# Performance work log

Measured on AMD Instinct MI355X. Metric: run time of the kernel, lower is better.

## Reference

```python
import jax, jax.numpy as jnp
import numpy as np

N = 50000
E = 600000
D = 128


def gcn_conv(x, row, col, w, W, b):
    """PyG GCNConv: add self-loops (weight 1), symmetric deg^-1/2 normalization,
    linear transform, edge-weighted scatter-add aggregation, then bias."""
    n = x.shape[0]
    loop = jnp.arange(n)
    r = jnp.concatenate([row, loop])            # source nodes, [E+N]
    c = jnp.concatenate([col, loop])            # target nodes, [E+N]
    ww = jnp.concatenate([w, jnp.ones((n,), x.dtype)])
    deg = jax.ops.segment_sum(ww, c, num_segments=n)          # weighted in-degree
    dinv = jnp.where(deg > 0, jax.lax.rsqrt(deg), jnp.zeros_like(deg))
    norm = dinv[r] * ww * dinv[c]               # [E+N]
    xl = x @ W                                  # [n, D_out]
    msg = norm[:, None] * xl[r]                 # gather + scale, [E+N, D_out]
    out = jax.ops.segment_sum(msg, c, num_segments=n)
    return out + b


def setup_inputs() -> dict:
    key = jax.random.key(0)
    ks = jax.random.split(key, 12)
    x = jax.random.normal(ks[0], (N, D), dtype=jnp.float32)
    edge_index = jax.random.randint(ks[1], (2, E), 0, N, dtype=jnp.int64)
    edge_weights = jax.random.uniform(ks[2], (E,), dtype=jnp.float32)
    s = 1.0 / np.sqrt(D)
    W1 = jax.random.uniform(ks[3], (D, D), jnp.float32, -s, s)
    b1 = jnp.zeros((D,), jnp.float32)
    W2 = jax.random.uniform(ks[4], (D, D), jnp.float32, -s, s)
    b2 = jnp.zeros((D,), jnp.float32)
    W3 = jax.random.uniform(ks[5], (D, D), jnp.float32, -s, s)
    b3 = jnp.zeros((D,), jnp.float32)
    prelu_w = jnp.array(0.25, jnp.float32)
    return {"x": x, "edge_index": edge_index, "edge_weights": edge_weights,
            "W1": W1, "b1": b1, "W2": W2, "b2": b2, "W3": W3, "b3": b3,
            "prelu_w": prelu_w}


def reference(x, edge_index, edge_weights, W1, b1, W2, b2, W3, b3, prelu_w):
    row, col = edge_index[0], edge_index[1]
    # layer 1: GCNConv -> (dropout: eval, identity) -> ELU
    h = gcn_conv(x, row, col, edge_weights, W1, b1)
    h = jax.nn.elu(h)
    # layer 2: GCNConv -> GELU (torch default = exact erf)
    h = gcn_conv(h, row, col, edge_weights, W2, b2)
    h = jax.nn.gelu(h, approximate=False)
    # layer 3: GCNConv -> PReLU (learnable scalar slope)
    h = gcn_conv(h, row, col, edge_weights, W3, b3)
    h = jnp.where(h >= 0, h, prelu_w * h)
    return h
```

## Files before the change

### kernel.cpp

```cpp
#include <hip/hip_runtime.h>
#include <hip/hip_fp16.h>
#include <math.h>

constexpr int D = 128;

struct __align__(16) H8 { __half2 h[4]; };
struct __align__(8)  H4 { __half2 a, b; };

typedef _Float16 half8 __attribute__((ext_vector_type(8)));
typedef float    floatx4 __attribute__((ext_vector_type(4)));


__device__ __forceinline__ int detect64(const int* __restrict__ ei) {
  int z = 0;
#pragma unroll
  for (int i = 0; i < 8; ++i) z |= ei[2 * i + 1];
  return (z == 0) ? 1 : 0;
}

__device__ __forceinline__ void load_edge(const int* __restrict__ ei, int e, int nE,
                                          int m64, int n, int& r, int& c) {
  if (m64) { r = ei[2 * (size_t)e]; c = ei[2 * ((size_t)nE + e)]; }
  else     { r = ei[(size_t)e];     c = ei[(size_t)nE + e]; }
  r = min(max(r, 0), n - 1);
  c = min(max(c, 0), n - 1);
}

__global__ void k_zero(int* __restrict__ cnt, int n) {
  int i = blockIdx.x * blockDim.x + threadIdx.x;
  if (i < n) cnt[i] = 0;
}

__global__ void k_pos(const int* __restrict__ ei, int* __restrict__ cnt,
                      int2* __restrict__ rc, int* __restrict__ pos, int nE, int n) {
  int e = blockIdx.x * blockDim.x + threadIdx.x;
  if (e >= nE) return;
  int m64 = detect64(ei);
  int r, c;
  load_edge(ei, e, nE, m64, n, r, c);
  rc[e] = make_int2(r, c);
  pos[e] = atomicAdd(&cnt[c], 1);
}

__global__ void k_scan1(const int* __restrict__ cnt, int* __restrict__ offs,
                        int* __restrict__ bsum, int n) {
  __shared__ int s[256];
  int t = threadIdx.x;
  int i = blockIdx.x * 256 + t;
  int v = (i < n) ? cnt[i] : 0;
  s[t] = v;
  __syncthreads();
  for (int off = 1; off < 256; off <<= 1) {
    int x = 0;
    if (t >= off) x = s[t - off];
    __syncthreads();
    if (t >= off) s[t] += x;
    __syncthreads();
  }
  if (i < n) offs[i] = s[t] - v;
  if (t == 255) bsum[blockIdx.x] = s[255];
}

__global__ void k_scan2(const int* __restrict__ bsum, int* __restrict__ boff, int nb) {
  __shared__ int s[256];
  int t = threadIdx.x;
  int v = (t < nb) ? bsum[t] : 0;
  s[t] = v;
  __syncthreads();
  for (int off = 1; off < 256; off <<= 1) {
    int x = 0;
    if (t >= off) x = s[t - off];
    __syncthreads();
    if (t >= off) s[t] += x;
    __syncthreads();
  }
  if (t < nb) boff[t] = s[t] - v;
}

__global__ void k_scan3(int* __restrict__ offs, const int* __restrict__ boff, int n, int nE) {
  int i = blockIdx.x * 256 + threadIdx.x;
  if (i < n) offs[i] += boff[blockIdx.x];
  if (i == 0) offs[n] = nE;
}

__global__ void k_fill(const int2* __restrict__ rc, const int* __restrict__ pos,
                       const float* __restrict__ w, const int* __restrict__ offs,
                       int2* __restrict__ ecf, int nE) {
  int e = blockIdx.x * blockDim.x + threadIdx.x;
  if (e >= nE) return;
  int2 p = rc[e];
  int idx = offs[p.y] + pos[e];
  ecf[idx] = make_int2(p.x, __float_as_int(w[e]));
}

__global__ void k_degdinv(const int2* __restrict__ ecf, const int* __restrict__ offs,
                          float* __restrict__ dinv, int n) {
  int i = blockIdx.x * blockDim.x + threadIdx.x;
  if (i >= n) return;
  float s = 1.0f;
  int e1 = offs[i + 1];
  for (int e = offs[i]; e < e1; ++e) s += __int_as_float(ecf[e].y);
  dinv[i] = rsqrtf(s);
}

__global__ void k_coef(const int2* __restrict__ ecf, const float* __restrict__ dinv,
                       unsigned int* __restrict__ ecf2, int nE) {
  int e = blockIdx.x * blockDim.x + threadIdx.x;
  if (e >= nE) return;
  int2 p = ecf[e];
  float c = dinv[p.x] * __int_as_float(p.y);
  ecf2[e] = ((unsigned int)p.x << 16) |
            (unsigned int)__half_as_ushort(__float2half_rn(c));
}

__global__ void k_wt(const float* __restrict__ W1, const float* __restrict__ W2,
                     const float* __restrict__ W3, __half* __restrict__ Wt) {
  __shared__ float s[128][129];
  const float* W = blockIdx.x == 0 ? W1 : (blockIdx.x == 1 ? W2 : W3);
  __half* o = Wt + (size_t)blockIdx.x * D * D;
  int tid = threadIdx.x;
#pragma unroll
  for (int i = 0; i < 16; ++i) {
    int flat = i * 1024 + tid * 4;
    int k = flat >> 7;
    int nn = flat & 127;
    float4 v = *(const float4*)(W + (size_t)k * D + nn);
    s[k][nn] = v.x; s[k][nn + 1] = v.y; s[k][nn + 2] = v.z; s[k][nn + 3] = v.w;
  }
  __syncthreads();
#pragma unroll
  for (int i = 0; i < 8; ++i) {
    int flat = i * 256 + tid;
    int nn = flat >> 4;
    int k0 = (flat & 15) * 8;
    H8 hv;
#pragma unroll
    for (int t = 0; t < 4; ++t)
      hv.h[t] = __floats2half2_rn(s[k0 + 2 * t][nn], s[k0 + 2 * t + 1][nn]);
    *(H8*)(o + (size_t)nn * D + k0) = hv;
  }
}

template <int ACT>
__device__ __forceinline__ float act_f(float x) {
  if (ACT == 1) return x > 0.f ? x : expm1f(x);
  if (ACT == 2) return 0.5f * x * (1.0f + erff(x * 0.70710678118654752440f));
  return x;
}

template <int ACT, typename AT>
__global__ __launch_bounds__(256) void k_gemm(const AT* __restrict__ A,
                                              const __half* __restrict__ Wt,
                                              __half* __restrict__ Y, int n) {
  const int wave = threadIdx.x >> 6;
  const int lane = threadIdx.x & 63;
  const int np = lane & 15;
  const int quad = lane >> 4;
  const int node = blockIdx.x * 64 + wave * 16 + np;
  const int nc = min(node, n - 1);

  half8 b[4];
#pragma unroll
  for (int s = 0; s < 4; ++s) {
    if constexpr (sizeof(AT) == 4) {
      const float* ap = (const float*)A + (size_t)nc * D + s * 32 + quad * 8;
      float4 v0 = *(const float4*)ap;
      float4 v1 = *(const float4*)(ap + 4);
      b[s][0] = (_Float16)act_f<ACT>(v0.x); b[s][1] = (_Float16)act_f<ACT>(v0.y);
      b[s][2] = (_Float16)act_f<ACT>(v0.z); b[s][3] = (_Float16)act_f<ACT>(v0.w);
      b[s][4] = (_Float16)act_f<ACT>(v1.x); b[s][5] = (_Float16)act_f<ACT>(v1.y);
      b[s][6] = (_Float16)act_f<ACT>(v1.z); b[s][7] = (_Float16)act_f<ACT>(v1.w);
    } else {
      half8 raw = *(const half8*)((const __half*)A + (size_t)nc * D + s * 32 + quad * 8);
#pragma unroll
      for (int t = 0; t < 8; ++t)
        b[s][t] = (_Float16)act_f<ACT>((float)raw[t]);
    }
  }

  floatx4 acc[8];
#pragma unroll
  for (int mt = 0; mt < 8; ++mt) acc[mt] = (floatx4){0.f, 0.f, 0.f, 0.f};

#pragma unroll
  for (int mt = 0; mt < 8; ++mt) {
#pragma unroll
    for (int s = 0; s < 4; ++s) {
      half8 a = *(const half8*)(Wt + (size_t)(mt * 16 + np) * D + s * 32 + quad * 8);
      acc[mt] = __builtin_amdgcn_mfma_f32_16x16x32_f16(a, b[s], acc[mt], 0, 0, 0);
    }
  }

  if (node < n) {
#pragma unroll
    for (int mt = 0; mt < 8; ++mt) {
      H4 hv;
      hv.a = __floats2half2_rn(acc[mt][0], acc[mt][1]);
      hv.b = __floats2half2_rn(acc[mt][2], acc[mt][3]);
      *(H4*)(Y + (size_t)node * D + mt * 16 + quad * 4) = hv;
    }
  }
}

__device__ __forceinline__ void fmacc8(float* acc, float c, const H8& y) {
  float2 f;
  f = __half22float2(y.h[0]); acc[0] += c * f.x; acc[1] += c * f.y;
  f = __half22float2(y.h[1]); acc[2] += c * f.x; acc[3] += c * f.y;
  f = __half22float2(y.h[2]); acc[4] += c * f.x; acc[5] += c * f.y;
  f = __half22float2(y.h[3]); acc[6] += c * f.x; acc[7] += c * f.y;
}

__device__ __forceinline__ float cdecode(unsigned int u) {
  return __half2float(__ushort_as_half((unsigned short)(u & 0xffffu)));
}

template <int PRELU, typename OutT>
__global__ __launch_bounds__(256) void k_agg(const __half* __restrict__ Y,
                                             const int* __restrict__ offs,
                                             const unsigned int* __restrict__ ecf2,
                                             const float* __restrict__ dinv,
                                             const float* __restrict__ bias,
                                             const float* __restrict__ pw,
                                             OutT* __restrict__ OUT, int n) {
  int gi = blockIdx.x * blockDim.x + threadIdx.x;
  int node = gi >> 5;
  int sub = (gi >> 4) & 1;
  int j = gi & 15;
  if (node >= n) return;
  float dc = dinv[node];
  float acc[8] = {0.f, 0.f, 0.f, 0.f, 0.f, 0.f, 0.f, 0.f};
  if (sub == 0) {
    H8 ys = *(const H8*)(Y + (size_t)node * D + j * 8);
    fmacc8(acc, dc, ys);
  }
  int e0 = offs[node], e1 = offs[node + 1];
  int e = e0 + sub;
  for (; e + 6 < e1; e += 8) {
    unsigned int u0 = ecf2[e], u1 = ecf2[e + 2], u2 = ecf2[e + 4], u3 = ecf2[e + 6];
    H8 y0 = *(const H8*)(Y + (size_t)(u0 >> 16) * D + j * 8);
    H8 y1 = *(const H8*)(Y + (size_t)(u1 >> 16) * D + j * 8);
    H8 y2 = *(const H8*)(Y + (size_t)(u2 >> 16) * D + j * 8);
    H8 y3 = *(const H8*)(Y + (size_t)(u3 >> 16) * D + j * 8);
    fmacc8(acc, cdecode(u0), y0);
    fmacc8(acc, cdecode(u1), y1);
    fmacc8(acc, cdecode(u2), y2);
    fmacc8(acc, cdecode(u3), y3);
  }
  for (; e < e1; e += 2) {
    unsigned int u = ecf2[e];
    H8 y = *(const H8*)(Y + (size_t)(u >> 16) * D + j * 8);
    fmacc8(acc, cdecode(u), y);
  }
#pragma unroll
  for (int i = 0; i < 8; ++i) acc[i] += __shfl_xor(acc[i], 16, 64);
  float4 b4 = *(const float4*)(bias + j * 8 + sub * 4);
  float o[4];
  o[0] = dc * acc[sub * 4 + 0] + b4.x;
  o[1] = dc * acc[sub * 4 + 1] + b4.y;
  o[2] = dc * acc[sub * 4 + 2] + b4.z;
  o[3] = dc * acc[sub * 4 + 3] + b4.w;
  if (PRELU) {
    float wv = *pw;
#pragma unroll
    for (int i = 0; i < 4; ++i) o[i] = o[i] >= 0.f ? o[i] : wv * o[i];
  }
  if constexpr (sizeof(OutT) == 4) {
    *(float4*)((float*)OUT + (size_t)node * D + j * 8 + sub * 4) =
        make_float4(o[0], o[1], o[2], o[3]);
  } else {
    H4 hv;
    hv.a = __floats2half2_rn(o[0], o[1]);
    hv.b = __floats2half2_rn(o[2], o[3]);
    *(H4*)((__half*)OUT + (size_t)node * D + j * 8 + sub * 4) = hv;
  }
}

extern "C" void kernel_launch(void* const* d_in, const int* in_sizes, int n_in,
                              void* d_out, int out_size, void* d_ws, size_t ws_size,
                              hipStream_t stream) {
  const float* x  = (const float*)d_in[0];
  const int*   ei = (const int*)d_in[1];
  const float* w  = (const float*)d_in[2];
  const float* W1 = (const float*)d_in[3];
  const float* b1 = (const float*)d_in[4];
  const float* W2 = (const float*)d_in[5];
  const float* b2 = (const float*)d_in[6];
  const float* W3 = (const float*)d_in[7];
  const float* b3 = (const float*)d_in[8];
  const float* pw = (const float*)d_in[9];
  const int N = in_sizes[0] / D;
  const int E = in_sizes[2];
  float* out = (float*)d_out;

  char* wsb = (char*)d_ws;
  size_t off = 0;
  auto alloc = [&](size_t bytes) {
    void* p = wsb + off;
    off = (off + bytes + 255) & ~(size_t)255;
    return p;
  };
  float*        dinv = (float*)alloc((size_t)N * 4);
  int*          cnt  = (int*)alloc((size_t)N * 4);
  int*          offs = (int*)alloc((size_t)(N + 1) * 4);
  int*          bsum = (int*)alloc(256 * 4);
  int*          boff = (int*)alloc(256 * 4);
  int2*         ecf  = (int2*)alloc((size_t)E * 8);
  unsigned int* ecf2 = (unsigned int*)alloc((size_t)E * 4);
  __half*       Wt   = (__half*)alloc((size_t)3 * D * D * 2);
  __half*       Y    = (__half*)alloc((size_t)N * D * 2);
  __half*       h    = (__half*)alloc((size_t)N * D * 2);
  int2*         rc   = (int2*)Y;
  int*          pos  = (int*)((char*)Y + (size_t)E * 8);

  const int nb = (N + 255) / 256;
  const int eb = (E + 255) / 256;

  hipLaunchKernelGGL(k_wt,      dim3(3),  dim3(256), 0, stream, W1, W2, W3, Wt);
  hipLaunchKernelGGL(k_zero,    dim3(nb), dim3(256), 0, stream, cnt, N);
  hipLaunchKernelGGL(k_pos,     dim3(eb), dim3(256), 0, stream, ei, cnt, rc, pos, E, N);
  hipLaunchKernelGGL(k_scan1,   dim3(nb), dim3(256), 0, stream, cnt, offs, bsum, N);
  hipLaunchKernelGGL(k_scan2,   dim3(1),  dim3(256), 0, stream, bsum, boff, nb);
  hipLaunchKernelGGL(k_scan3,   dim3(nb), dim3(256), 0, stream, offs, boff, N, E);
  hipLaunchKernelGGL(k_fill,    dim3(eb), dim3(256), 0, stream, rc, pos, w, offs, ecf, E);
  hipLaunchKernelGGL(k_degdinv, dim3(nb), dim3(256), 0, stream, ecf, offs, dinv, N);
  hipLaunchKernelGGL(k_coef,    dim3(eb), dim3(256), 0, stream, ecf, dinv, ecf2, E);

  const int gb = (N + 63) / 64;
  const int ab = (N * 32 + 255) / 256;

  hipLaunchKernelGGL((k_gemm<0, float>),  dim3(gb), dim3(256), 0, stream, x, Wt,             Y, N);
  hipLaunchKernelGGL((k_agg<0, __half>),  dim3(ab), dim3(256), 0, stream, Y, offs, ecf2, dinv, b1, pw, h, N);
  hipLaunchKernelGGL((k_gemm<1, __half>), dim3(gb), dim3(256), 0, stream, h, Wt + D * D,     Y, N);
  hipLaunchKernelGGL((k_agg<0, __half>),  dim3(ab), dim3(256), 0, stream, Y, offs, ecf2, dinv, b2, pw, h, N);
  hipLaunchKernelGGL((k_gemm<2, __half>), dim3(gb), dim3(256), 0, stream, h, Wt + 2 * D * D, Y, N);
  hipLaunchKernelGGL((k_agg<1, float>),   dim3(ab), dim3(256), 0, stream, Y, offs, ecf2, dinv, b3, pw, out, N);
}
```

Baseline: 307.4 us.

## Split feature matrices into 32-column chunks for cache-friendly aggregation

Stores the transformed features Y and the hidden activations h in a chunked layout of four 32-feature slabs, each holding all nodes. Each aggregation block now handles one chunk for 32 nodes, so the random gathers in a block touch only one 3.2 MB slab instead of the whole 12.8 MB matrix. The aim is better L2 hit rate on the gather-heavy aggregation. In exchange, edge indices and coefficients are reread four times, and each gathered row is only 64 bytes.

```diff
diff --git a/kernel.cpp b/kernel.cpp
--- a/kernel.cpp
+++ b/kernel.cpp
@@ -171,7 +171,7 @@
       b[s][4] = (_Float16)act_f<ACT>(v1.x); b[s][5] = (_Float16)act_f<ACT>(v1.y);
       b[s][6] = (_Float16)act_f<ACT>(v1.z); b[s][7] = (_Float16)act_f<ACT>(v1.w);
     } else {
-      half8 raw = *(const half8*)((const __half*)A + (size_t)nc * D + s * 32 + quad * 8);
+      half8 raw = *(const half8*)((const __half*)A + ((size_t)s * n + nc) * 32 + quad * 8);
 #pragma unroll
       for (int t = 0; t < 8; ++t)
         b[s][t] = (_Float16)act_f<ACT>((float)raw[t]);
@@ -197,7 +197,8 @@
       H4 hv;
       hv.a = __floats2half2_rn(acc[mt][0], acc[mt][1]);
       hv.b = __floats2half2_rn(acc[mt][2], acc[mt][3]);
-      *(H4*)(Y + (size_t)node * D + mt * 16 + quad * 4) = hv;
+      int f0 = mt * 16 + quad * 4;
+      *(H4*)(Y + ((size_t)(f0 >> 5) * n + node) * 32 + (f0 & 31)) = hv;
     }
   }
 }
@@ -222,25 +223,27 @@
                                              const float* __restrict__ bias,
                                              const float* __restrict__ pw,
                                              OutT* __restrict__ OUT, int n) {
-  int gi = blockIdx.x * blockDim.x + threadIdx.x;
-  int node = gi >> 5;
-  int sub = (gi >> 4) & 1;
-  int j = gi & 15;
+  const int chunk = blockIdx.x & 3;
+  const int t = threadIdx.x;
+  const int node = (blockIdx.x >> 2) * 32 + (t >> 3);
+  const int sub = (t >> 2) & 1;
+  const int j = t & 3;
   if (node >= n) return;
+  const __half* Yc = Y + (size_t)chunk * n * 32;
   float dc = dinv[node];
   float acc[8] = {0.f, 0.f, 0.f, 0.f, 0.f, 0.f, 0.f, 0.f};
   if (sub == 0) {
-    H8 ys = *(const H8*)(Y + (size_t)node * D + j * 8);
+    H8 ys = *(const H8*)(Yc + (size_t)node * 32 + j * 8);
     fmacc8(acc, dc, ys);
   }
   int e0 = offs[node], e1 = offs[node + 1];
   int e = e0 + sub;
   for (; e + 6 < e1; e += 8) {
     unsigned int u0 = ecf2[e], u1 = ecf2[e + 2], u2 = ecf2[e + 4], u3 = ecf2[e + 6];
-    H8 y0 = *(const H8*)(Y + (size_t)(u0 >> 16) * D + j * 8);
-    H8 y1 = *(const H8*)(Y + (size_t)(u1 >> 16) * D + j * 8);
-    H8 y2 = *(const H8*)(Y + (size_t)(u2 >> 16) * D + j * 8);
-    H8 y3 = *(const H8*)(Y + (size_t)(u3 >> 16) * D + j * 8);
+    H8 y0 = *(const H8*)(Yc + (size_t)(u0 >> 16) * 32 + j * 8);
+    H8 y1 = *(const H8*)(Yc + (size_t)(u1 >> 16) * 32 + j * 8);
+    H8 y2 = *(const H8*)(Yc + (size_t)(u2 >> 16) * 32 + j * 8);
+    H8 y3 = *(const H8*)(Yc + (size_t)(u3 >> 16) * 32 + j * 8);
     fmacc8(acc, cdecode(u0), y0);
     fmacc8(acc, cdecode(u1), y1);
     fmacc8(acc, cdecode(u2), y2);
@@ -248,12 +251,12 @@
   }
   for (; e < e1; e += 2) {
     unsigned int u = ecf2[e];
-    H8 y = *(const H8*)(Y + (size_t)(u >> 16) * D + j * 8);
+    H8 y = *(const H8*)(Yc + (size_t)(u >> 16) * 32 + j * 8);
     fmacc8(acc, cdecode(u), y);
   }
 #pragma unroll
-  for (int i = 0; i < 8; ++i) acc[i] += __shfl_xor(acc[i], 16, 64);
-  float4 b4 = *(const float4*)(bias + j * 8 + sub * 4);
+  for (int i = 0; i < 8; ++i) acc[i] += __shfl_xor(acc[i], 4, 64);
+  float4 b4 = *(const float4*)(bias + chunk * 32 + j * 8 + sub * 4);
   float o[4];
   o[0] = dc * acc[sub * 4 + 0] + b4.x;
   o[1] = dc * acc[sub * 4 + 1] + b4.y;
@@ -265,13 +268,13 @@
     for (int i = 0; i < 4; ++i) o[i] = o[i] >= 0.f ? o[i] : wv * o[i];
   }
   if constexpr (sizeof(OutT) == 4) {
-    *(float4*)((float*)OUT + (size_t)node * D + j * 8 + sub * 4) =
+    *(float4*)((float*)OUT + (size_t)node * D + chunk * 32 + j * 8 + sub * 4) =
         make_float4(o[0], o[1], o[2], o[3]);
   } else {
     H4 hv;
     hv.a = __floats2half2_rn(o[0], o[1]);
     hv.b = __floats2half2_rn(o[2], o[3]);
-    *(H4*)((__half*)OUT + (size_t)node * D + j * 8 + sub * 4) = hv;
+    *(H4*)((__half*)OUT + ((size_t)chunk * n + node) * 32 + j * 8 + sub * 4) = hv;
   }
 }
 
@@ -326,7 +329,7 @@
   hipLaunchKernelGGL(k_coef,    dim3(eb), dim3(256), 0, stream, ecf, dinv, ecf2, E);
 
   const int gb = (N + 63) / 64;
-  const int ab = (N * 32 + 255) / 256;
+  const int ab = 4 * ((N + 31) / 32);
 
   hipLaunchKernelGGL((k_gemm<0, float>),  dim3(gb), dim3(256), 0, stream, x, Wt,             Y, N);
   hipLaunchKernelGGL((k_agg<0, __half>),  dim3(ab), dim3(256), 0, stream, Y, offs, ecf2, dinv, b1, pw, h, N);
```

Result: faster. 300.5 us (-2.2%).
